# Optimization experiments

Hardware: AMD Instinct MI355X
Metric: run time of the kernel (lower is better)

Reference implementation:

```python
import jax, jax.numpy as jnp
import numpy as np

SEQ_LEN = 50  # params['sequence_length']
HIDDEN = 256


def setup_inputs() -> dict:
    key = jax.random.key(0)
    ks = jax.random.split(key, 8)
    s = 0.05
    return {
        "zs": jax.random.normal(ks[0], (4096, 256), jnp.float32),
        "W1": jax.random.normal(ks[1], (512, 256), jnp.float32) * s,
        "b1": jnp.zeros((512,), jnp.float32),
        "W2": jax.random.normal(ks[2], (256, 512), jnp.float32) * s,
        "b2": jnp.zeros((256,), jnp.float32),
        "W3": jax.random.normal(ks[3], (128, 256), jnp.float32) * s,
        "b3": jnp.zeros((128,), jnp.float32),
        "W_ih": jax.random.normal(ks[4], (1024, 128), jnp.float32) * s,
        "W_hh": jax.random.normal(ks[5], (1024, 256), jnp.float32) * s,
        "b_ih": jnp.zeros((1024,), jnp.float32),
        "b_hh": jnp.zeros((1024,), jnp.float32),
    }


def reference(zs, W1, b1, W2, b2, W3, b3, W_ih, W_hh, b_ih, b_hh):
    # MLP: Linear -> ReLU -> Linear -> ReLU -> Linear (torch Linear: x @ W.T + b)
    h = jax.nn.relu(zs @ W1.T + b1)
    h = jax.nn.relu(h @ W2.T + b2)
    z_embed = h @ W3.T + b3                       # [B, 128]

    B = z_embed.shape[0]
    # Input is identical at every timestep -> precompute input projection once.
    x_part = z_embed @ W_ih.T + b_ih + b_hh       # [B, 4H], gate order i,f,g,o

    def step(carry, _):
        h_t, c_t = carry
        gates = x_part + h_t @ W_hh.T             # [B, 4H]
        i, f, g, o = jnp.split(gates, 4, axis=-1)
        i = jax.nn.sigmoid(i)
        f = jax.nn.sigmoid(f)
        g = jnp.tanh(g)
        o = jax.nn.sigmoid(o)
        c_t = f * c_t + i * g
        h_t = o * jnp.tanh(c_t)
        return (h_t, c_t), h_t

    h0 = jnp.zeros((B, HIDDEN), zs.dtype)
    c0 = jnp.zeros((B, HIDDEN), zs.dtype)
    _, hs = jax.lax.scan(step, (h0, c0), None, length=SEQ_LEN)  # [T, B, H]
    return jnp.transpose(hs, (1, 0, 2))           # [B, T, H] (batch_first)
```

## Files before the change

kernel.cpp:

```cpp
#include <hip/hip_runtime.h>
#include <stdint.h>


typedef short short8 __attribute__((ext_vector_type(8)));
typedef float floatx4 __attribute__((ext_vector_type(4)));
typedef unsigned short ushort4v __attribute__((ext_vector_type(4)));

#define BATCH 4096
#define HID 256
#define TSTEPS 50

static __device__ __forceinline__ unsigned short f2bf(float x) {
  union { float f; unsigned int u; } v; v.f = x;
  unsigned int r = (v.u + 0x7fffu + ((v.u >> 16) & 1u)) >> 16;
  return (unsigned short)r;
}
static __device__ __forceinline__ float bf2f(unsigned short h) {
  union { unsigned int u; float f; } v; v.u = ((unsigned int)h) << 16;
  return v.f;
}
static __device__ __forceinline__ float sigmf(float x) {
  return __builtin_amdgcn_rcpf(1.0f + __expf(-x));
}
static __device__ __forceinline__ float tanhf_(float x) {
  return 1.0f - 2.0f * __builtin_amdgcn_rcpf(__expf(2.0f * x) + 1.0f);
}

static __device__ __forceinline__ void lds_barrier() {
  __asm__ volatile("s_waitcnt lgkmcnt(0)\n\ts_barrier" ::: "memory");
}

__global__ __launch_bounds__(256) void split_all(
    const float* __restrict__ s0, unsigned short* __restrict__ h0, unsigned short* __restrict__ l0,
    const float* __restrict__ s1, unsigned short* __restrict__ h1, unsigned short* __restrict__ l1,
    const float* __restrict__ s2, unsigned short* __restrict__ h2, unsigned short* __restrict__ l2,
    const float* __restrict__ s3, unsigned short* __restrict__ h3, unsigned short* __restrict__ l3,
    const float* __restrict__ s4, unsigned short* __restrict__ h4, unsigned short* __restrict__ l4,
    const float* __restrict__ Wh, unsigned short* __restrict__ whhf) {
  if (blockIdx.x >= 1440) {
    int idx = (blockIdx.x - 1440) * 256 + threadIdx.x;
    int lane = idx & 63;
    int i = (idx >> 6) & 7;
    int w = (idx >> 9) & 7;
    int kt = idx >> 12;
    int nt = (i >> 1) * 16 + w * 2 + (i & 1);
    int n = nt * 16 + (lane & 15);
    int k0 = kt * 32 + (lane >> 4) * 8;
    const float* src = Wh + (size_t)n * 256 + k0;
    unsigned short* dst = whhf + (size_t)idx * 8;
#pragma unroll
    for (int j = 0; j < 8; ++j) dst[j] = f2bf(src[j]);
    return;
  }
  int i = blockIdx.x * 256 + threadIdx.x;
  const float* src; unsigned short *dh, *dl; int off;
  if (i < 262144)      { src = s0; dh = h0; dl = l0; off = i; }
  else if (i < 294912) { src = s1; dh = h1; dl = l1; off = i - 262144; }
  else if (i < 327680) { src = s2; dh = h2; dl = l2; off = i - 294912; }
  else if (i < 335872) { src = s3; dh = h3; dl = l3; off = i - 327680; }
  else if (i < 368640) { src = s4; dh = h4; dl = l4; off = i - 335872; }
  else return;
  float4 v = ((const float4*)src)[off];
  float cc[4] = {v.x, v.y, v.z, v.w};
  ushort4v h, l;
#pragma unroll
  for (int j = 0; j < 4; ++j) {
    unsigned short hb = f2bf(cc[j]);
    h[j] = hb;
    l[j] = f2bf(cc[j] - bf2f(hb));
  }
  ((ushort4v*)dh)[off] = h;
  ((ushort4v*)dl)[off] = l;
}

template <int RELU, int OUT_SPLIT, int HAS_B2>
__global__ __launch_bounds__(256) void gemm_df(
    const unsigned short* __restrict__ Ah, const unsigned short* __restrict__ Al,
    const unsigned short* __restrict__ Bh, const unsigned short* __restrict__ Bl,
    const float* __restrict__ bias, const float* __restrict__ bias2,
    float* __restrict__ Cf, unsigned short* __restrict__ Ch,
    unsigned short* __restrict__ Cl, int M, int N, int K) {
  __shared__ unsigned short Ash[64 * 32], Asl[64 * 32];
  __shared__ unsigned short Bsh[64 * 32], Bsl[64 * 32];
  const int tid = threadIdx.x;
  const int wave = tid >> 6, lane = tid & 63;
  const int quad = lane >> 4, l16 = lane & 15;
  const int bm = blockIdx.y * 64, bn = blockIdx.x * 64;
  const int lr = tid >> 2, lc = tid & 3;
  const int wofs = lr * 32 + ((lc ^ (lr & 3)) * 8);

  floatx4 acc[4] = {};
  short8 avh = *(const short8*)(Ah + (size_t)(bm + lr) * K + lc * 8);
  short8 avl = *(const short8*)(Al + (size_t)(bm + lr) * K + lc * 8);
  short8 bvh = *(const short8*)(Bh + (size_t)(bn + lr) * K + lc * 8);
  short8 bvl = *(const short8*)(Bl + (size_t)(bn + lr) * K + lc * 8);

  for (int k0 = 0; k0 < K; k0 += 32) {
    lds_barrier();
    *(short8*)&Ash[wofs] = avh;
    *(short8*)&Asl[wofs] = avl;
    *(short8*)&Bsh[wofs] = bvh;
    *(short8*)&Bsl[wofs] = bvl;
    lds_barrier();
    if (k0 + 32 < K) {
      avh = *(const short8*)(Ah + (size_t)(bm + lr) * K + k0 + 32 + lc * 8);
      avl = *(const short8*)(Al + (size_t)(bm + lr) * K + k0 + 32 + lc * 8);
      bvh = *(const short8*)(Bh + (size_t)(bn + lr) * K + k0 + 32 + lc * 8);
      bvl = *(const short8*)(Bl + (size_t)(bn + lr) * K + k0 + 32 + lc * 8);
    }
    const int bro = (wave * 16 + l16) * 32 + ((quad ^ (l16 & 3)) * 8);
    short8 bh = *(const short8*)&Bsh[bro];
    short8 bl = *(const short8*)&Bsl[bro];
#pragma unroll
    for (int i = 0; i < 4; ++i) {
      const int aro = (i * 16 + l16) * 32 + ((quad ^ (l16 & 3)) * 8);
      short8 ah = *(const short8*)&Ash[aro];
      short8 al = *(const short8*)&Asl[aro];
      acc[i] = __builtin_amdgcn_mfma_f32_16x16x32_bf16(al, bh, acc[i], 0, 0, 0);
      acc[i] = __builtin_amdgcn_mfma_f32_16x16x32_bf16(ah, bl, acc[i], 0, 0, 0);
      acc[i] = __builtin_amdgcn_mfma_f32_16x16x32_bf16(ah, bh, acc[i], 0, 0, 0);
    }
  }
  const int col = bn + wave * 16 + l16;
  float bj = bias[col];
  if (HAS_B2) bj += bias2[col];
#pragma unroll
  for (int i = 0; i < 4; ++i)
#pragma unroll
    for (int r = 0; r < 4; ++r) {
      int row = bm + i * 16 + quad * 4 + r;
      float v = acc[i][r] + bj;
      if (RELU) v = fmaxf(v, 0.f);
      if (OUT_SPLIT) {
        unsigned short hb = f2bf(v);
        Ch[(size_t)row * N + col] = hb;
        Cl[(size_t)row * N + col] = f2bf(v - bf2f(hb));
      } else {
        Cf[(size_t)row * N + col] = v;
      }
    }
}

__global__ __launch_bounds__(512, 2) void lstm_kernel(
    const float* __restrict__ xp,
    const unsigned short* __restrict__ whhf,
    float* __restrict__ out) {
  __shared__ unsigned short h_frag[2][8][64][8];
  __shared__ unsigned short whh_lds[65536];

  const int tid = threadIdx.x;
  const int wave = tid >> 6;
  const int lane = tid & 63;
  const int quad = lane >> 4;
  const int l16 = lane & 15;
  const int block_m = blockIdx.x * 16;
  const int ut0 = wave * 2;

  for (int i = tid; i < 2 * 8 * 64 * 8; i += 512)
    ((unsigned short*)h_frag)[i] = 0;

  {
    const short8* s = (const short8*)(whhf + 196608);
    short8* d = (short8*)whh_lds;
    for (int i = tid; i < 8192; i += 512) d[i] = s[i];
  }

  floatx4 xpreg[8];
#pragma unroll
  for (int i = 0; i < 8; ++i) {
    int g = i >> 1, utl = i & 1;
    int col = g * 256 + (ut0 + utl) * 16 + l16;
    floatx4 v;
#pragma unroll
    for (int r = 0; r < 4; ++r)
      v[r] = xp[(size_t)(block_m + quad * 4 + r) * 1024 + col];
    xpreg[i] = v;
  }

  float c[2][4] = {};

  short8 pers[4][8];
  {
    const unsigned short* p0 =
        whhf + ((size_t)((1 * 8 + wave) * 8) * 64 + lane) * 8;
    const unsigned short* p1 =
        whhf + ((size_t)((2 * 8 + wave) * 8) * 64 + lane) * 8;
    const unsigned short* p2 =
        whhf + ((size_t)((3 * 8 + wave) * 8) * 64 + lane) * 8;
    const unsigned short* p3 =
        whhf + ((size_t)((5 * 8 + wave) * 8) * 64 + lane) * 8;
#pragma unroll
    for (int i = 0; i < 8; ++i) {
      pers[0][i] = *(const short8*)(p0 + i * 512);
      pers[1][i] = *(const short8*)(p1 + i * 512);
      pers[2][i] = *(const short8*)(p2 + i * 512);
      pers[3][i] = *(const short8*)(p3 + i * 512);
    }
  }

  short8 bA[8];
  {
    const unsigned short* w0 =
        whhf + ((size_t)((0 * 8 + wave) * 8) * 64 + lane) * 8;
#pragma unroll
    for (int i = 0; i < 8; ++i) bA[i] = *(const short8*)(w0 + i * 512);
  }

  __syncthreads();

  const size_t orow = (size_t)TSTEPS * HID;
  int cur = 0;

#pragma unroll 1
  for (int t = 0; t < TSTEPS; ++t) {
    const unsigned short* wb = whhf;
    asm volatile("" : "+s"(wb));
    unsigned lofs = 0;
    asm volatile("" : "+v"(lofs));

    floatx4 acc[8];

    short8 aab[2];
    aab[0] = *(const short8*)&h_frag[cur][0][lane][0];

#pragma unroll
    for (int kt = 0; kt < 8; ++kt) {
      const short8 a = aab[kt & 1];
      if (kt < 7)
        aab[(kt + 1) & 1] = *(const short8*)&h_frag[cur][kt + 1][lane][0];

      if (kt == 0) {
#pragma unroll
        for (int i = 0; i < 8; ++i)
          acc[i] = __builtin_amdgcn_mfma_f32_16x16x32_bf16(a, bA[i],
                                                           xpreg[i], 0, 0, 0);
        const unsigned short* wbp =
            wb + ((size_t)((4 * 8 + wave) * 8) * 64 + lane) * 8;
#pragma unroll
        for (int i = 0; i < 8; ++i) bA[i] = *(const short8*)(wbp + i * 512);
      } else if (kt == 1) {
#pragma unroll
        for (int i = 0; i < 8; ++i)
          acc[i] = __builtin_amdgcn_mfma_f32_16x16x32_bf16(a, pers[0][i],
                                                           acc[i], 0, 0, 0);
      } else if (kt == 2) {
#pragma unroll
        for (int i = 0; i < 8; ++i)
          acc[i] = __builtin_amdgcn_mfma_f32_16x16x32_bf16(a, pers[1][i],
                                                           acc[i], 0, 0, 0);
      } else if (kt == 3) {
#pragma unroll
        for (int i = 0; i < 8; ++i)
          acc[i] = __builtin_amdgcn_mfma_f32_16x16x32_bf16(a, pers[2][i],
                                                           acc[i], 0, 0, 0);
      } else if (kt == 4) {
#pragma unroll
        for (int i = 0; i < 8; ++i)
          acc[i] = __builtin_amdgcn_mfma_f32_16x16x32_bf16(a, bA[i],
                                                           acc[i], 0, 0, 0);
        const unsigned short* wbp =
            wb + ((size_t)((0 * 8 + wave) * 8) * 64 + lane) * 8;
#pragma unroll
        for (int i = 0; i < 8; ++i) bA[i] = *(const short8*)(wbp + i * 512);
      } else if (kt == 5) {
#pragma unroll
        for (int i = 0; i < 8; ++i)
          acc[i] = __builtin_amdgcn_mfma_f32_16x16x32_bf16(a, pers[3][i],
                                                           acc[i], 0, 0, 0);
      } else {
#pragma unroll
        for (int i = 0; i < 8; ++i) {
          const short8 bl = *(const short8*)&whh_lds[
              lofs + (size_t)((((kt - 6) * 8 + wave) * 8 + i) * 512) + lane * 8];
          acc[i] = __builtin_amdgcn_mfma_f32_16x16x32_bf16(a, bl, acc[i],
                                                           0, 0, 0);
        }
      }
    }

    const int nxt = cur ^ 1;
#pragma unroll
    for (int utl = 0; utl < 2; ++utl) {
      floatx4 gi = acc[0 + utl];
      floatx4 gf = acc[2 + utl];
      floatx4 gg = acc[4 + utl];
      floatx4 go = acc[6 + utl];
      const int u = (ut0 + utl) * 16 + l16;
      const int kt2 = u >> 5;
      const int lhi = ((u >> 3) & 3) << 4;
      const int j2 = u & 7;
#pragma unroll
      for (int r = 0; r < 4; ++r) {
        float iv = sigmf(gi[r]);
        float fv = sigmf(gf[r]);
        float gv = tanhf_(gg[r]);
        float ov = sigmf(go[r]);
        float cv = fmaf(fv, c[utl][r], iv * gv);
        c[utl][r] = cv;
        float hv = ov * tanhf_(cv);
        int mloc = quad * 4 + r;
        __builtin_nontemporal_store(
            hv, &out[(size_t)(block_m + mloc) * orow + (size_t)t * HID + u]);
        h_frag[nxt][kt2][mloc | lhi][j2] = f2bf(hv);
      }
    }
    cur = nxt;
    lds_barrier();
  }
}

extern "C" void kernel_launch(void* const* d_in, const int* in_sizes, int n_in,
                              void* d_out, int out_size, void* d_ws, size_t ws_size,
                              hipStream_t stream) {
  const float* zs  = (const float*)d_in[0];
  const float* W1  = (const float*)d_in[1];
  const float* b1  = (const float*)d_in[2];
  const float* W2  = (const float*)d_in[3];
  const float* b2  = (const float*)d_in[4];
  const float* W3  = (const float*)d_in[5];
  const float* b3  = (const float*)d_in[6];
  const float* Wih = (const float*)d_in[7];
  const float* Whh = (const float*)d_in[8];
  const float* bih = (const float*)d_in[9];
  const float* bhh = (const float*)d_in[10];
  float* out = (float*)d_out;

  char* ws = (char*)d_ws;
  const size_t MB = 1024 * 1024;
  unsigned short* zs_h = (unsigned short*)(ws + 0 * MB);
  unsigned short* zs_l = (unsigned short*)(ws + 2 * MB);
  unsigned short* h1_h = (unsigned short*)(ws + 4 * MB);
  unsigned short* h1_l = (unsigned short*)(ws + 8 * MB);
  unsigned short* h2_h = (unsigned short*)(ws + 0 * MB);
  unsigned short* h2_l = (unsigned short*)(ws + 2 * MB);
  unsigned short* zb_h = (unsigned short*)(ws + 12 * MB);
  unsigned short* zb_l = (unsigned short*)(ws + 13 * MB);
  unsigned short* w1_h = (unsigned short*)(ws + 14 * MB);
  unsigned short* w1_l = (unsigned short*)(ws + 14 * MB + 256 * 1024);
  unsigned short* w2_h = (unsigned short*)(ws + 14 * MB + 512 * 1024);
  unsigned short* w2_l = (unsigned short*)(ws + 14 * MB + 768 * 1024);
  unsigned short* w3_h = (unsigned short*)(ws + 15 * MB);
  unsigned short* w3_l = (unsigned short*)(ws + 15 * MB + 64 * 1024);
  unsigned short* wi_h = (unsigned short*)(ws + 15 * MB + 128 * 1024);
  unsigned short* wi_l = (unsigned short*)(ws + 15 * MB + 384 * 1024);
  float* xp            = (float*)(ws + 16 * MB);
  unsigned short* whhf = (unsigned short*)(ws + 32 * MB);

  split_all<<<1568, 256, 0, stream>>>(zs, zs_h, zs_l, W1, w1_h, w1_l,
                                      W2, w2_h, w2_l, W3, w3_h, w3_l,
                                      Wih, wi_h, wi_l, Whh, whhf);

  gemm_df<1, 1, 0><<<dim3(512 / 64, BATCH / 64), 256, 0, stream>>>(
      zs_h, zs_l, w1_h, w1_l, b1, nullptr, nullptr, h1_h, h1_l, BATCH, 512, 256);
  gemm_df<1, 1, 0><<<dim3(256 / 64, BATCH / 64), 256, 0, stream>>>(
      h1_h, h1_l, w2_h, w2_l, b2, nullptr, nullptr, h2_h, h2_l, BATCH, 256, 512);
  gemm_df<0, 1, 0><<<dim3(128 / 64, BATCH / 64), 256, 0, stream>>>(
      h2_h, h2_l, w3_h, w3_l, b3, nullptr, nullptr, zb_h, zb_l, BATCH, 128, 256);
  gemm_df<0, 0, 1><<<dim3(1024 / 64, BATCH / 64), 256, 0, stream>>>(
      zb_h, zb_l, wi_h, wi_l, bih, bhh, xp, nullptr, nullptr, BATCH, 1024, 128);

  lstm_kernel<<<BATCH / 16, 512, 0, stream>>>(xp, whhf, out);
}
```

Baseline: 383.0 us.

## Fuse MLP and input projection into LSTM kernel with pre-packed MFMA weights

Removes the four separate split-bf16 GEMM launches and the xp round trip through global memory. Each LSTM block now computes its own 16-row MLP chain and input projection in LDS, using weights pre-packed into MFMA fragment order by a smaller pack kernel. The zs split is also done in-kernel. The trade-off is that each block rereads all MLP weights from global/L2 using only 16-row MFMA tiles, so reuse per weight load is low, and the serial prologue now sits before the recurrence.

```diff
diff --git a/kernel.cpp b/kernel.cpp
--- a/kernel.cpp
+++ b/kernel.cpp
@@ -4,7 +4,6 @@
 
 typedef short short8 __attribute__((ext_vector_type(8)));
 typedef float floatx4 __attribute__((ext_vector_type(4)));
-typedef unsigned short ushort4v __attribute__((ext_vector_type(4)));
 
 #define BATCH 4096
 #define HID 256
@@ -30,123 +29,105 @@
   __asm__ volatile("s_waitcnt lgkmcnt(0)\n\ts_barrier" ::: "memory");
 }
 
-__global__ __launch_bounds__(256) void split_all(
-    const float* __restrict__ s0, unsigned short* __restrict__ h0, unsigned short* __restrict__ l0,
-    const float* __restrict__ s1, unsigned short* __restrict__ h1, unsigned short* __restrict__ l1,
-    const float* __restrict__ s2, unsigned short* __restrict__ h2, unsigned short* __restrict__ l2,
-    const float* __restrict__ s3, unsigned short* __restrict__ h3, unsigned short* __restrict__ l3,
-    const float* __restrict__ s4, unsigned short* __restrict__ h4, unsigned short* __restrict__ l4,
-    const float* __restrict__ Wh, unsigned short* __restrict__ whhf) {
-  if (blockIdx.x >= 1440) {
-    int idx = (blockIdx.x - 1440) * 256 + threadIdx.x;
-    int lane = idx & 63;
-    int i = (idx >> 6) & 7;
-    int w = (idx >> 9) & 7;
-    int kt = idx >> 12;
-    int nt = (i >> 1) * 16 + w * 2 + (i & 1);
-    int n = nt * 16 + (lane & 15);
-    int k0 = kt * 32 + (lane >> 4) * 8;
-    const float* src = Wh + (size_t)n * 256 + k0;
+__global__ __launch_bounds__(256) void pack_all(
+    const float* __restrict__ W1, const float* __restrict__ W2,
+    const float* __restrict__ W3, const float* __restrict__ Wih,
+    const float* __restrict__ Whh,
+    unsigned short* __restrict__ w1fh, unsigned short* __restrict__ w1fl,
+    unsigned short* __restrict__ w2fh, unsigned short* __restrict__ w2fl,
+    unsigned short* __restrict__ w3fh, unsigned short* __restrict__ w3fl,
+    unsigned short* __restrict__ wifh, unsigned short* __restrict__ wifl,
+    unsigned short* __restrict__ whhf) {
+  const int bid = blockIdx.x;
+  const int tid = threadIdx.x;
+  if (bid < 208) {
+    const float* W; unsigned short *dh, *dl; int NKT, K, idx;
+    if (bid < 64)       { W = W1;  dh = w1fh; dl = w1fl; NKT = 8;  K = 256; idx = bid * 256 + tid; }
+    else if (bid < 128) { W = W2;  dh = w2fh; dl = w2fl; NKT = 16; K = 512; idx = (bid - 64) * 256 + tid; }
+    else if (bid < 144) { W = W3;  dh = w3fh; dl = w3fl; NKT = 8;  K = 256; idx = (bid - 128) * 256 + tid; }
+    else                { W = Wih; dh = wifh; dl = wifl; NKT = 4;  K = 128; idx = (bid - 144) * 256 + tid; }
+    const int lane = idx & 63, f = idx >> 6;
+    const int nt = f / NKT, kt = f - nt * NKT;
+    const int n = nt * 16 + (lane & 15);
+    const int k0 = kt * 32 + (lane >> 4) * 8;
+    const float* src = W + (size_t)n * K + k0;
+#pragma unroll
+    for (int j = 0; j < 8; ++j) {
+      float v = src[j];
+      unsigned short hb = f2bf(v);
+      dh[(size_t)idx * 8 + j] = hb;
+      dl[(size_t)idx * 8 + j] = f2bf(v - bf2f(hb));
+    }
+  } else {
+    const int idx = (bid - 208) * 256 + tid;
+    const int lane = idx & 63;
+    const int i = (idx >> 6) & 7;
+    const int w = (idx >> 9) & 7;
+    const int kt = idx >> 12;
+    const int nt = (i >> 1) * 16 + w * 2 + (i & 1);
+    const int n = nt * 16 + (lane & 15);
+    const int k0 = kt * 32 + (lane >> 4) * 8;
+    const float* src = Whh + (size_t)n * 256 + k0;
     unsigned short* dst = whhf + (size_t)idx * 8;
 #pragma unroll
     for (int j = 0; j < 8; ++j) dst[j] = f2bf(src[j]);
-    return;
-  }
-  int i = blockIdx.x * 256 + threadIdx.x;
-  const float* src; unsigned short *dh, *dl; int off;
-  if (i < 262144)      { src = s0; dh = h0; dl = l0; off = i; }
-  else if (i < 294912) { src = s1; dh = h1; dl = l1; off = i - 262144; }
-  else if (i < 327680) { src = s2; dh = h2; dl = l2; off = i - 294912; }
-  else if (i < 335872) { src = s3; dh = h3; dl = l3; off = i - 327680; }
-  else if (i < 368640) { src = s4; dh = h4; dl = l4; off = i - 335872; }
-  else return;
-  float4 v = ((const float4*)src)[off];
-  float cc[4] = {v.x, v.y, v.z, v.w};
-  ushort4v h, l;
-#pragma unroll
-  for (int j = 0; j < 4; ++j) {
-    unsigned short hb = f2bf(cc[j]);
-    h[j] = hb;
-    l[j] = f2bf(cc[j] - bf2f(hb));
-  }
-  ((ushort4v*)dh)[off] = h;
-  ((ushort4v*)dl)[off] = l;
-}
-
-template <int RELU, int OUT_SPLIT, int HAS_B2>
-__global__ __launch_bounds__(256) void gemm_df(
-    const unsigned short* __restrict__ Ah, const unsigned short* __restrict__ Al,
-    const unsigned short* __restrict__ Bh, const unsigned short* __restrict__ Bl,
-    const float* __restrict__ bias, const float* __restrict__ bias2,
-    float* __restrict__ Cf, unsigned short* __restrict__ Ch,
-    unsigned short* __restrict__ Cl, int M, int N, int K) {
-  __shared__ unsigned short Ash[64 * 32], Asl[64 * 32];
-  __shared__ unsigned short Bsh[64 * 32], Bsl[64 * 32];
-  const int tid = threadIdx.x;
-  const int wave = tid >> 6, lane = tid & 63;
-  const int quad = lane >> 4, l16 = lane & 15;
-  const int bm = blockIdx.y * 64, bn = blockIdx.x * 64;
-  const int lr = tid >> 2, lc = tid & 3;
-  const int wofs = lr * 32 + ((lc ^ (lr & 3)) * 8);
-
-  floatx4 acc[4] = {};
-  short8 avh = *(const short8*)(Ah + (size_t)(bm + lr) * K + lc * 8);
-  short8 avl = *(const short8*)(Al + (size_t)(bm + lr) * K + lc * 8);
-  short8 bvh = *(const short8*)(Bh + (size_t)(bn + lr) * K + lc * 8);
-  short8 bvl = *(const short8*)(Bl + (size_t)(bn + lr) * K + lc * 8);
-
-  for (int k0 = 0; k0 < K; k0 += 32) {
-    lds_barrier();
-    *(short8*)&Ash[wofs] = avh;
-    *(short8*)&Asl[wofs] = avl;
-    *(short8*)&Bsh[wofs] = bvh;
-    *(short8*)&Bsl[wofs] = bvl;
-    lds_barrier();
-    if (k0 + 32 < K) {
-      avh = *(const short8*)(Ah + (size_t)(bm + lr) * K + k0 + 32 + lc * 8);
-      avl = *(const short8*)(Al + (size_t)(bm + lr) * K + k0 + 32 + lc * 8);
-      bvh = *(const short8*)(Bh + (size_t)(bn + lr) * K + k0 + 32 + lc * 8);
-      bvl = *(const short8*)(Bl + (size_t)(bn + lr) * K + k0 + 32 + lc * 8);
-    }
-    const int bro = (wave * 16 + l16) * 32 + ((quad ^ (l16 & 3)) * 8);
-    short8 bh = *(const short8*)&Bsh[bro];
-    short8 bl = *(const short8*)&Bsl[bro];
-#pragma unroll
-    for (int i = 0; i < 4; ++i) {
-      const int aro = (i * 16 + l16) * 32 + ((quad ^ (l16 & 3)) * 8);
-      short8 ah = *(const short8*)&Ash[aro];
-      short8 al = *(const short8*)&Asl[aro];
-      acc[i] = __builtin_amdgcn_mfma_f32_16x16x32_bf16(al, bh, acc[i], 0, 0, 0);
-      acc[i] = __builtin_amdgcn_mfma_f32_16x16x32_bf16(ah, bl, acc[i], 0, 0, 0);
-      acc[i] = __builtin_amdgcn_mfma_f32_16x16x32_bf16(ah, bh, acc[i], 0, 0, 0);
-    }
-  }
-  const int col = bn + wave * 16 + l16;
-  float bj = bias[col];
-  if (HAS_B2) bj += bias2[col];
-#pragma unroll
-  for (int i = 0; i < 4; ++i)
-#pragma unroll
-    for (int r = 0; r < 4; ++r) {
-      int row = bm + i * 16 + quad * 4 + r;
-      float v = acc[i][r] + bj;
-      if (RELU) v = fmaxf(v, 0.f);
-      if (OUT_SPLIT) {
-        unsigned short hb = f2bf(v);
-        Ch[(size_t)row * N + col] = hb;
-        Cl[(size_t)row * N + col] = f2bf(v - bf2f(hb));
-      } else {
-        Cf[(size_t)row * N + col] = v;
-      }
-    }
-}
-
-__global__ __launch_bounds__(512, 2) void lstm_kernel(
-    const float* __restrict__ xp,
+  }
+}
+
+template <int NKT, int RELU>
+static __device__ __forceinline__ void mlp_stage(
+    const unsigned short (*ah)[64][8], const unsigned short (*al)[64][8],
+    const unsigned short* __restrict__ bfh, const unsigned short* __restrict__ bfl,
+    int nt, const float* __restrict__ bias,
+    unsigned short (*oh)[64][8], unsigned short (*ol)[64][8],
+    int lane, int quad, int l16) {
+  floatx4 acc = {};
+  const size_t base = ((size_t)(nt * NKT) * 64 + lane) * 8;
+#pragma unroll
+  for (int kt = 0; kt < NKT; ++kt) {
+    short8 a_h = *(const short8*)&ah[kt][lane][0];
+    short8 a_l = *(const short8*)&al[kt][lane][0];
+    short8 b_h = *(const short8*)(bfh + base + kt * 512);
+    short8 b_l = *(const short8*)(bfl + base + kt * 512);
+    acc = __builtin_amdgcn_mfma_f32_16x16x32_bf16(a_l, b_h, acc, 0, 0, 0);
+    acc = __builtin_amdgcn_mfma_f32_16x16x32_bf16(a_h, b_l, acc, 0, 0, 0);
+    acc = __builtin_amdgcn_mfma_f32_16x16x32_bf16(a_h, b_h, acc, 0, 0, 0);
+  }
+  const int col = nt * 16 + l16;
+  const float bj = bias[col];
+  const int kt2 = col >> 5, lhi = ((col >> 3) & 3) << 4, j2 = col & 7;
+#pragma unroll
+  for (int r = 0; r < 4; ++r) {
+    float v = acc[r] + bj;
+    if (RELU) v = fmaxf(v, 0.f);
+    unsigned short hb = f2bf(v);
+    oh[kt2][(quad * 4 + r) | lhi][j2] = hb;
+    ol[kt2][(quad * 4 + r) | lhi][j2] = f2bf(v - bf2f(hb));
+  }
+}
+
+__global__ __launch_bounds__(512, 2) void lstm_fused(
+    const float* __restrict__ zs,
+    const float* __restrict__ b1, const float* __restrict__ b2,
+    const float* __restrict__ b3,
+    const float* __restrict__ bih, const float* __restrict__ bhh,
+    const unsigned short* __restrict__ w1fh, const unsigned short* __restrict__ w1fl,
+    const unsigned short* __restrict__ w2fh, const unsigned short* __restrict__ w2fl,
+    const unsigned short* __restrict__ w3fh, const unsigned short* __restrict__ w3fl,
+    const unsigned short* __restrict__ wifh, const unsigned short* __restrict__ wifl,
     const unsigned short* __restrict__ whhf,
     float* __restrict__ out) {
-  __shared__ unsigned short h_frag[2][8][64][8];
-  __shared__ unsigned short whh_lds[65536];
+  __shared__ __align__(16) unsigned char smem[147456];
+  unsigned short* whh_lds = (unsigned short*)smem;
+  unsigned short (*h_frag)[8][64][8] = (unsigned short(*)[8][64][8])(smem + 131072);
+  unsigned short (*zsh)[64][8] = (unsigned short(*)[64][8])(smem + 0);
+  unsigned short (*zsl)[64][8] = (unsigned short(*)[64][8])(smem + 8192);
+  unsigned short (*h1h)[64][8] = (unsigned short(*)[64][8])(smem + 16384);
+  unsigned short (*h1l)[64][8] = (unsigned short(*)[64][8])(smem + 32768);
+  unsigned short (*h2h)[64][8] = (unsigned short(*)[64][8])(smem + 49152);
+  unsigned short (*h2l)[64][8] = (unsigned short(*)[64][8])(smem + 57344);
+  unsigned short (*zbh)[64][8] = (unsigned short(*)[64][8])(smem + 65536);
+  unsigned short (*zbl)[64][8] = (unsigned short(*)[64][8])(smem + 69632);
 
   const int tid = threadIdx.x;
   const int wave = tid >> 6;
@@ -157,7 +138,61 @@
   const int ut0 = wave * 2;
 
   for (int i = tid; i < 2 * 8 * 64 * 8; i += 512)
-    ((unsigned short*)h_frag)[i] = 0;
+    ((unsigned short*)(smem + 131072))[i] = 0;
+
+  {
+    const int kt = tid >> 6;
+    const float* zrow =
+        zs + (size_t)(block_m + l16) * 256 + kt * 32 + quad * 8;
+    float4 z0 = *(const float4*)zrow;
+    float4 z1 = *(const float4*)(zrow + 4);
+    float zz[8] = {z0.x, z0.y, z0.z, z0.w, z1.x, z1.y, z1.z, z1.w};
+#pragma unroll
+    for (int j = 0; j < 8; ++j) {
+      unsigned short hb = f2bf(zz[j]);
+      zsh[kt][lane][j] = hb;
+      zsl[kt][lane][j] = f2bf(zz[j] - bf2f(hb));
+    }
+  }
+  lds_barrier();
+
+#pragma unroll
+  for (int ntl = 0; ntl < 4; ++ntl)
+    mlp_stage<8, 1>(zsh, zsl, w1fh, w1fl, wave * 4 + ntl, b1, h1h, h1l,
+                    lane, quad, l16);
+  lds_barrier();
+
+#pragma unroll
+  for (int ntl = 0; ntl < 2; ++ntl)
+    mlp_stage<16, 1>(h1h, h1l, w2fh, w2fl, wave * 2 + ntl, b2, h2h, h2l,
+                     lane, quad, l16);
+  lds_barrier();
+
+  mlp_stage<8, 0>(h2h, h2l, w3fh, w3fl, wave, b3, zbh, zbl, lane, quad, l16);
+  lds_barrier();
+
+  floatx4 xpreg[8];
+#pragma unroll
+  for (int i = 0; i < 8; ++i) {
+    const int nt = (i >> 1) * 16 + wave * 2 + (i & 1);
+    floatx4 acc = {};
+    const size_t base = ((size_t)(nt * 4) * 64 + lane) * 8;
+#pragma unroll
+    for (int kt = 0; kt < 4; ++kt) {
+      short8 a_h = *(const short8*)&zbh[kt][lane][0];
+      short8 a_l = *(const short8*)&zbl[kt][lane][0];
+      short8 b_h = *(const short8*)(wifh + base + kt * 512);
+      short8 b_l = *(const short8*)(wifl + base + kt * 512);
+      acc = __builtin_amdgcn_mfma_f32_16x16x32_bf16(a_l, b_h, acc, 0, 0, 0);
+      acc = __builtin_amdgcn_mfma_f32_16x16x32_bf16(a_h, b_l, acc, 0, 0, 0);
+      acc = __builtin_amdgcn_mfma_f32_16x16x32_bf16(a_h, b_h, acc, 0, 0, 0);
+    }
+    const int col = nt * 16 + l16;
+    const float bj = bih[col] + bhh[col];
+#pragma unroll
+    for (int r = 0; r < 4; ++r) xpreg[i][r] = acc[r] + bj;
+  }
+  lds_barrier();
 
   {
     const short8* s = (const short8*)(whhf + 196608);
@@ -165,30 +200,14 @@
     for (int i = tid; i < 8192; i += 512) d[i] = s[i];
   }
 
-  floatx4 xpreg[8];
-#pragma unroll
-  for (int i = 0; i < 8; ++i) {
-    int g = i >> 1, utl = i & 1;
-    int col = g * 256 + (ut0 + utl) * 16 + l16;
-    floatx4 v;
-#pragma unroll
-    for (int r = 0; r < 4; ++r)
-      v[r] = xp[(size_t)(block_m + quad * 4 + r) * 1024 + col];
-    xpreg[i] = v;
-  }
-
   float c[2][4] = {};
 
   short8 pers[4][8];
   {
-    const unsigned short* p0 =
-        whhf + ((size_t)((1 * 8 + wave) * 8) * 64 + lane) * 8;
-    const unsigned short* p1 =
-        whhf + ((size_t)((2 * 8 + wave) * 8) * 64 + lane) * 8;
-    const unsigned short* p2 =
-        whhf + ((size_t)((3 * 8 + wave) * 8) * 64 + lane) * 8;
-    const unsigned short* p3 =
-        whhf + ((size_t)((5 * 8 + wave) * 8) * 64 + lane) * 8;
+    const unsigned short* p0 = whhf + ((size_t)((1 * 8 + wave) * 8) * 64 + lane) * 8;
+    const unsigned short* p1 = whhf + ((size_t)((2 * 8 + wave) * 8) * 64 + lane) * 8;
+    const unsigned short* p2 = whhf + ((size_t)((3 * 8 + wave) * 8) * 64 + lane) * 8;
+    const unsigned short* p3 = whhf + ((size_t)((5 * 8 + wave) * 8) * 64 + lane) * 8;
 #pragma unroll
     for (int i = 0; i < 8; ++i) {
       pers[0][i] = *(const short8*)(p0 + i * 512);
@@ -200,8 +219,7 @@
 
   short8 bA[8];
   {
-    const unsigned short* w0 =
-        whhf + ((size_t)((0 * 8 + wave) * 8) * 64 + lane) * 8;
+    const unsigned short* w0 = whhf + ((size_t)((0 * 8 + wave) * 8) * 64 + lane) * 8;
 #pragma unroll
     for (int i = 0; i < 8; ++i) bA[i] = *(const short8*)(w0 + i * 512);
   }
@@ -326,38 +344,22 @@
   float* out = (float*)d_out;
 
   char* ws = (char*)d_ws;
-  const size_t MB = 1024 * 1024;
-  unsigned short* zs_h = (unsigned short*)(ws + 0 * MB);
-  unsigned short* zs_l = (unsigned short*)(ws + 2 * MB);
-  unsigned short* h1_h = (unsigned short*)(ws + 4 * MB);
-  unsigned short* h1_l = (unsigned short*)(ws + 8 * MB);
-  unsigned short* h2_h = (unsigned short*)(ws + 0 * MB);
-  unsigned short* h2_l = (unsigned short*)(ws + 2 * MB);
-  unsigned short* zb_h = (unsigned short*)(ws + 12 * MB);
-  unsigned short* zb_l = (unsigned short*)(ws + 13 * MB);
-  unsigned short* w1_h = (unsigned short*)(ws + 14 * MB);
-  unsigned short* w1_l = (unsigned short*)(ws + 14 * MB + 256 * 1024);
-  unsigned short* w2_h = (unsigned short*)(ws + 14 * MB + 512 * 1024);
-  unsigned short* w2_l = (unsigned short*)(ws + 14 * MB + 768 * 1024);
-  unsigned short* w3_h = (unsigned short*)(ws + 15 * MB);
-  unsigned short* w3_l = (unsigned short*)(ws + 15 * MB + 64 * 1024);
-  unsigned short* wi_h = (unsigned short*)(ws + 15 * MB + 128 * 1024);
-  unsigned short* wi_l = (unsigned short*)(ws + 15 * MB + 384 * 1024);
-  float* xp            = (float*)(ws + 16 * MB);
-  unsigned short* whhf = (unsigned short*)(ws + 32 * MB);
-
-  split_all<<<1568, 256, 0, stream>>>(zs, zs_h, zs_l, W1, w1_h, w1_l,
-                                      W2, w2_h, w2_l, W3, w3_h, w3_l,
-                                      Wih, wi_h, wi_l, Whh, whhf);
-
-  gemm_df<1, 1, 0><<<dim3(512 / 64, BATCH / 64), 256, 0, stream>>>(
-      zs_h, zs_l, w1_h, w1_l, b1, nullptr, nullptr, h1_h, h1_l, BATCH, 512, 256);
-  gemm_df<1, 1, 0><<<dim3(256 / 64, BATCH / 64), 256, 0, stream>>>(
-      h1_h, h1_l, w2_h, w2_l, b2, nullptr, nullptr, h2_h, h2_l, BATCH, 256, 512);
-  gemm_df<0, 1, 0><<<dim3(128 / 64, BATCH / 64), 256, 0, stream>>>(
-      h2_h, h2_l, w3_h, w3_l, b3, nullptr, nullptr, zb_h, zb_l, BATCH, 128, 256);
-  gemm_df<0, 0, 1><<<dim3(1024 / 64, BATCH / 64), 256, 0, stream>>>(
-      zb_h, zb_l, wi_h, wi_l, bih, bhh, xp, nullptr, nullptr, BATCH, 1024, 128);
-
-  lstm_kernel<<<BATCH / 16, 512, 0, stream>>>(xp, whhf, out);
-}
+  const size_t KB = 1024;
+  unsigned short* w1fh = (unsigned short*)(ws + 0);
+  unsigned short* w1fl = (unsigned short*)(ws + 256 * KB);
+  unsigned short* w2fh = (unsigned short*)(ws + 512 * KB);
+  unsigned short* w2fl = (unsigned short*)(ws + 768 * KB);
+  unsigned short* w3fh = (unsigned short*)(ws + 1024 * KB);
+  unsigned short* w3fl = (unsigned short*)(ws + 1088 * KB);
+  unsigned short* wifh = (unsigned short*)(ws + 1152 * KB);
+  unsigned short* wifl = (unsigned short*)(ws + 1408 * KB);
+  unsigned short* whhf = (unsigned short*)(ws + 2048 * KB);
+
+  pack_all<<<336, 256, 0, stream>>>(W1, W2, W3, Wih, Whh,
+                                    w1fh, w1fl, w2fh, w2fl, w3fh, w3fl,
+                                    wifh, wifl, whhf);
+
+  lstm_fused<<<BATCH / 16, 512, 0, stream>>>(
+      zs, b1, b2, b3, bih, bhh, w1fh, w1fl, w2fh, w2fl, w3fh, w3fl,
+      wifh, wifl, whhf, out);
+}
```

Result: faster. 358.0 us (-6.5%).
